# Performance work log

Measured on AMD Instinct MI355X. Metric: run time of the kernel, lower is better.

## Reference

```python
import jax, jax.numpy as jnp
import numpy as np

B, NSV, NTRK, K, H = 512, 128, 512, 8, 16


def setup_inputs() -> dict:
    key = jax.random.key(0)
    ks = jax.random.split(key, 12)
    p = lambda k, shp: (jax.random.normal(k, shp, dtype=jnp.float32) * 0.1)
    return {
        "x_sv": jax.random.normal(ks[0], (B * NSV, 2), dtype=jnp.float32),
        "x_trk": jax.random.normal(ks[1], (B * NTRK, 8), dtype=jnp.float32),
        "batch_sv": jnp.repeat(jnp.arange(B, dtype=jnp.int32), NSV),
        "batch_trk": jnp.repeat(jnp.arange(B, dtype=jnp.int32), NTRK),
        # sv_encode: Linear(2,16) -> ELU -> Linear(16,16)
        "W1s": p(ks[2], (2, H)), "b1s": jnp.zeros((H,), jnp.float32),
        "W2s": p(ks[3], (H, H)), "b2s": jnp.zeros((H,), jnp.float32),
        # trk_encode: Linear(8,16) -> ELU -> Linear(16,16)
        "W1t": p(ks[4], (8, H)), "b1t": jnp.zeros((H,), jnp.float32),
        "W2t": p(ks[5], (H, H)), "b2t": jnp.zeros((H,), jnp.float32),
        # edge MLP: Linear(2*16, 16)
        "We": p(ks[6], (2 * H, H)), "be": jnp.zeros((H,), jnp.float32),
        # output head: Linear(16, 1)
        "Wo": p(ks[7], (H, 1)), "bo": jnp.zeros((1,), jnp.float32),
    }


def reference(x_sv, x_trk, batch_sv, batch_trk,
              W1s, b1s, W2s, b2s, W1t, b1t, W2t, b2t, We, be, Wo, bo):
    # Node encoders
    sv = jax.nn.elu(x_sv @ W1s + b1s) @ W2s + b2s      # [Nsv, H]
    trk = jax.nn.elu(x_trk @ W1t + b1t) @ W2t + b2t    # [Ntrk, H]

    # Regular batching: reshape to per-event blocks (batch_sv/batch_trk are
    # contiguous repeats of arange(B) with NSV / NTRK nodes per event).
    svb = sv.reshape(B, NSV, H)      # [B, S, H]
    trkb = trk.reshape(B, NTRK, H)   # [B, T, H]

    # kNN in encoded space: squared L2 distance per event, k nearest SVs per track
    t_sq = jnp.sum(trkb * trkb, -1)[:, :, None]          # [B, T, 1]
    s_sq = jnp.sum(svb * svb, -1)[:, None, :]            # [B, 1, S]
    dots = jnp.einsum("bth,bsh->bts", trkb, svb)         # [B, T, S]
    d2 = t_sq + s_sq - 2.0 * dots                        # [B, T, S]
    _, idx = jax.lax.top_k(-d2, K)                       # [B, T, K] indices into S

    # Gather neighbor SV features: [B, T, K, H]
    nbr = jax.vmap(lambda s, i: s[i])(svb, idx)

    # EdgeConv message: nn(cat[x_i, x_j - x_i]), x_i = track (target), x_j = SV
    ti = trkb[:, :, None, :]                                    # [B, T, 1, H]
    msg_in = jnp.concatenate(
        [jnp.broadcast_to(ti, nbr.shape), nbr - ti], axis=-1)   # [B, T, K, 2H]
    msg = msg_in @ We + be                                      # [B, T, K, H]
    feats = jnp.max(msg, axis=2).reshape(B * NTRK, H)           # max aggregation

    # Output head + per-event average pool (avg_pool_x with cluster == batch)
    out = jax.nn.sigmoid(feats @ Wo + bo)                       # [Ntrk, 1]
    sums = jax.ops.segment_sum(out, batch_trk, num_segments=B)  # [B, 1]
    cnts = jax.ops.segment_sum(jnp.ones_like(out), batch_trk, num_segments=B)
    pooled = sums / cnts                                        # [B, 1]
    batch_out = jnp.arange(B, dtype=jnp.int32)
    return pooled, batch_out
```

## Files before the change

### kernel.cpp

```cpp
#include <hip/hip_runtime.h>
#include <cmath>

#define BB   512
#define NSV  128
#define NTRK 512
#define KK   8
#define HH   16
#define TPB  1024
#define RSTR 20
#define PSTR 20
#define KSTR 17

typedef float vf2 __attribute__((ext_vector_type(2)));

__device__ __forceinline__ float elu_f(float x) {
    return x > 0.0f ? x : expm1f(x);
}
__device__ __forceinline__ unsigned umin_u(unsigned a, unsigned b) { return a < b ? a : b; }
__device__ __forceinline__ unsigned med3u(unsigned a, unsigned b, unsigned c) {
    unsigned d;
    asm("v_med3_u32 %0, %1, %2, %3" : "=v"(d) : "v"(a), "v"(b), "v"(c));
    return d;
}

__global__ __launch_bounds__(TPB, 8) void fused_all(
    const float* __restrict__ x_sv, const float* __restrict__ x_trk,
    const float* __restrict__ W1s, const float* __restrict__ b1s,
    const float* __restrict__ W2s, const float* __restrict__ b2s,
    const float* __restrict__ W1t, const float* __restrict__ b1t,
    const float* __restrict__ W2t, const float* __restrict__ b2t,
    const float* __restrict__ We,  const float* __restrict__ be,
    const float* __restrict__ Wo,  const float* __restrict__ bo,
    float* __restrict__ svw,
    const float* __restrict__ svr,
    float* __restrict__ out)
{
    __shared__ float    proj[NSV][PSTR];
    __shared__ unsigned kbuf[NTRK][KSTR];
    __shared__ float    ucS[HH + 1];
    __shared__ float    sred[TPB / 64];

    const int b   = blockIdx.x, tid = threadIdx.x;
    const int tl  = tid & 511;
    const int sh  = __builtin_amdgcn_readfirstlane(tid >> 9);

    if (tid < NSV) {
        const float* xp = x_sv + (size_t)(b * NSV + tid) * 2;
        float x0 = xp[0], x1 = xp[1];
        float hb[HH];
        #pragma unroll
        for (int h = 0; h < HH; ++h)
            hb[h] = elu_f(x0 * W1s[h] + x1 * W1s[HH + h] + b1s[h]);
        float o[HH], sq = 0.0f;
        #pragma unroll
        for (int h2 = 0; h2 < HH; ++h2) {
            float a = b2s[h2];
            #pragma unroll
            for (int h = 0; h < HH; ++h) a += hb[h] * W2s[h * HH + h2];
            o[h2] = a;
            sq += a * a;
        }
        float* dst = svw + (size_t)(b * NSV + tid) * RSTR;
        #pragma unroll
        for (int h4 = 0; h4 < 4; ++h4)
            *(float4*)&dst[h4 * 4] = make_float4(o[h4*4], o[h4*4+1], o[h4*4+2], o[h4*4+3]);
        dst[HH] = 0.5f * sq;
        #pragma unroll
        for (int h = 0; h < HH; ++h) {
            float a = 0.0f;
            #pragma unroll
            for (int j = 0; j < HH; ++j) a += o[j] * We[(HH + j) * HH + h];
            proj[tid][h] = a;
        }
    } else if (tid < NSV + HH) {
        int j = tid - NSV;
        float a = 0.0f;
        #pragma unroll
        for (int h = 0; h < HH; ++h)
            a += (We[j * HH + h] - We[(HH + j) * HH + h]) * Wo[h];
        ucS[j] = a;
    } else if (tid == NSV + HH) {
        float a = bo[0];
        #pragma unroll
        for (int h = 0; h < HH; ++h) a += be[h] * Wo[h];
        ucS[HH] = a;
    }

    float tf[HH], htsq;
    vf2 ntfp[8];
    {
        const float* xp = x_trk + (size_t)(b * NTRK + tl) * 8;
        float x[8];
        *(float4*)&x[0] = *(const float4*)&xp[0];
        *(float4*)&x[4] = *(const float4*)&xp[4];
        float hb[HH];
        #pragma unroll
        for (int h = 0; h < HH; ++h) {
            float a = b1t[h];
            #pragma unroll
            for (int i = 0; i < 8; ++i) a += x[i] * W1t[i * HH + h];
            hb[h] = elu_f(a);
        }
        float sq = 0.0f;
        #pragma unroll
        for (int h2 = 0; h2 < HH; ++h2) {
            float a = b2t[h2];
            #pragma unroll
            for (int h = 0; h < HH; ++h) a += hb[h] * W2t[h * HH + h2];
            tf[h2] = a;
            sq += a * a;
        }
        htsq = 0.5f * sq;
        #pragma unroll
        for (int j = 0; j < 8; ++j) {
            vf2 t; t.x = -tf[2 * j]; t.y = -tf[2 * j + 1];
            ntfp[j] = t;
        }
    }

    unsigned k[KK];
    #pragma unroll
    for (int q = 0; q < KK; ++q) k[q] = 0xFFFFFFFFu;

    __syncthreads();

    const int sbase = sh * 64;
    const float* rp = svr + (size_t)(b * NSV + sbase) * RSTR;

    vf2 pa[8], pb[8]; float ha, hbv;

    #define LOADROW(buf, hv, idx)                                      \
        do {                                                           \
            const float* _r = rp + (size_t)(idx) * RSTR;               \
            _Pragma("unroll")                                          \
            for (int _j = 0; _j < 8; ++_j)                             \
                buf[_j] = *(const vf2*)(_r + 2 * _j);                  \
            hv = _r[HH];                                               \
        } while (0)

    #define BODY(buf, hv, idx)                                         \
        do {                                                           \
            vf2 a0 = ntfp[0] * buf[0];                                 \
            vf2 a1 = ntfp[1] * buf[1];                                 \
            vf2 a2 = ntfp[2] * buf[2];                                 \
            vf2 a3 = ntfp[3] * buf[3];                                 \
            a0 = __builtin_elementwise_fma(ntfp[4], buf[4], a0);       \
            a1 = __builtin_elementwise_fma(ntfp[5], buf[5], a1);       \
            a2 = __builtin_elementwise_fma(ntfp[6], buf[6], a2);       \
            a3 = __builtin_elementwise_fma(ntfp[7], buf[7], a3);       \
            a0 = a0 + a1; a2 = a2 + a3; a0 = a0 + a2;                  \
            float e = fmaxf((htsq + hv) + (a0.x + a0.y), 0.0f);        \
            unsigned v = (__float_as_uint(e) & 0xFFFFFF80u)            \
                         | (unsigned)(sbase + (idx));                  \
            unsigned nk0 = umin_u(v, k[0]);                            \
            unsigned nk1 = med3u(v, k[0], k[1]);                       \
            unsigned nk2 = med3u(v, k[1], k[2]);                       \
            unsigned nk3 = med3u(v, k[2], k[3]);                       \
            unsigned nk4 = med3u(v, k[3], k[4]);                       \
            unsigned nk5 = med3u(v, k[4], k[5]);                       \
            unsigned nk6 = med3u(v, k[5], k[6]);                       \
            unsigned nk7 = med3u(v, k[6], k[7]);                       \
            k[0] = nk0; k[1] = nk1; k[2] = nk2; k[3] = nk3;            \
            k[4] = nk4; k[5] = nk5; k[6] = nk6; k[7] = nk7;            \
        } while (0)

    LOADROW(pa, ha, 0);
    LOADROW(pb, hbv, 1);
    for (int s = 0; s < 64 - 2; s += 2) {
        BODY(pa, ha, s);
        LOADROW(pa, ha, s + 2);
        BODY(pb, hbv, s + 1);
        LOADROW(pb, hbv, s + 3);
    }
    BODY(pa, ha, 62);
    BODY(pb, hbv, 63);

    #undef LOADROW
    #undef BODY

    #pragma unroll
    for (int q = 0; q < KK; ++q) kbuf[tl][sh * 8 + q] = k[q];
    __syncthreads();

    unsigned m[KK];
    {
        const unsigned* pk = &kbuf[tl][(sh ^ 1) * 8];
        #pragma unroll
        for (int i = 0; i < KK; ++i) m[i] = umin_u(k[i], pk[7 - i]);
    }

    float local;
    {
        float acc = ucS[HH];
        #pragma unroll
        for (int j = 0; j < HH; ++j) acc = fmaf(tf[j], ucS[j], acc);

        float mx[HH];
        #pragma unroll
        for (int h = 0; h < HH; ++h) mx[h] = -INFINITY;
        #pragma unroll
        for (int q = 0; q < KK; ++q) {
            const float* pr = &proj[m[q] & 127u][0];
            #pragma unroll
            for (int h4 = 0; h4 < 4; ++h4) {
                float4 p = *(const float4*)&pr[h4 * 4];
                mx[h4 * 4 + 0] = fmaxf(mx[h4 * 4 + 0], p.x);
                mx[h4 * 4 + 1] = fmaxf(mx[h4 * 4 + 1], p.y);
                mx[h4 * 4 + 2] = fmaxf(mx[h4 * 4 + 2], p.z);
                mx[h4 * 4 + 3] = fmaxf(mx[h4 * 4 + 3], p.w);
            }
        }
        #pragma unroll
        for (int h = 0; h < HH; ++h) acc = fmaf(mx[h], Wo[h], acc);
        local = 1.0f / (1.0f + expf(-acc));
    }

    #pragma unroll
    for (int off = 32; off > 0; off >>= 1)
        local += __shfl_down(local, off, 64);
    if ((tid & 63) == 0) sred[tid >> 6] = local;
    __syncthreads();
    if (tid == 0) {
        float tot = 0.0f;
        #pragma unroll
        for (int w = 0; w < TPB / 64; ++w) tot += sred[w];
        out[b]      = tot * (1.0f / (2 * NTRK));
        out[BB + b] = (float)b;
    }
}

extern "C" void kernel_launch(void* const* d_in, const int* in_sizes, int n_in,
                              void* d_out, int out_size, void* d_ws, size_t ws_size,
                              hipStream_t stream) {
    const float* x_sv  = (const float*)d_in[0];
    const float* x_trk = (const float*)d_in[1];
    const float* W1s = (const float*)d_in[4];
    const float* b1s = (const float*)d_in[5];
    const float* W2s = (const float*)d_in[6];
    const float* b2s = (const float*)d_in[7];
    const float* W1t = (const float*)d_in[8];
    const float* b1t = (const float*)d_in[9];
    const float* W2t = (const float*)d_in[10];
    const float* b2t = (const float*)d_in[11];
    const float* We  = (const float*)d_in[12];
    const float* be  = (const float*)d_in[13];
    const float* Wo  = (const float*)d_in[14];
    const float* bo  = (const float*)d_in[15];
    float* out = (float*)d_out;

    float* rows = (float*)d_ws;

    fused_all<<<BB, TPB, 0, stream>>>(x_sv, x_trk,
                                      W1s, b1s, W2s, b2s,
                                      W1t, b1t, W2t, b2t,
                                      We, be, Wo, bo,
                                      rows, rows, out);
}
```

Measured before the change: 131.1 us.

## Split each event across two blocks with four SV segments and merge networks

```diff
diff --git a/kernel.cpp b/kernel.cpp
--- a/kernel.cpp
+++ b/kernel.cpp
@@ -7,9 +7,12 @@
 #define KK   8
 #define HH   16
 #define TPB  1024
+#define TRB  256
+#define SEGN 32
 #define RSTR 20
 #define PSTR 20
-#define KSTR 17
+#define TSTR 18
+#define KBS  25
 
 typedef float vf2 __attribute__((ext_vector_type(2)));
 
@@ -17,10 +20,26 @@
     return x > 0.0f ? x : expm1f(x);
 }
 __device__ __forceinline__ unsigned umin_u(unsigned a, unsigned b) { return a < b ? a : b; }
+__device__ __forceinline__ unsigned umax_u(unsigned a, unsigned b) { return a > b ? a : b; }
 __device__ __forceinline__ unsigned med3u(unsigned a, unsigned b, unsigned c) {
     unsigned d;
     asm("v_med3_u32 %0, %1, %2, %3" : "=v"(d) : "v"(a), "v"(b), "v"(c));
     return d;
+}
+__device__ __forceinline__ void ceu(unsigned& a, unsigned& b) {
+    unsigned lo = umin_u(a, b), hi = umax_u(a, b);
+    a = lo; b = hi;
+}
+__device__ __forceinline__ void merge8(unsigned* a, const unsigned* b) {
+    unsigned s[8];
+    #pragma unroll
+    for (int i = 0; i < 8; ++i) s[i] = umin_u(a[i], b[7 - i]);
+    #pragma unroll
+    for (int i = 0; i < 4; ++i) ceu(s[i], s[i + 4]);
+    ceu(s[0], s[2]); ceu(s[1], s[3]); ceu(s[4], s[6]); ceu(s[5], s[7]);
+    ceu(s[0], s[1]); ceu(s[2], s[3]); ceu(s[4], s[5]); ceu(s[6], s[7]);
+    #pragma unroll
+    for (int i = 0; i < 8; ++i) a[i] = s[i];
 }
 
 __global__ __launch_bounds__(TPB, 8) void fused_all(
@@ -33,16 +52,20 @@
     const float* __restrict__ Wo,  const float* __restrict__ bo,
     float* __restrict__ svw,
     const float* __restrict__ svr,
+    float* __restrict__ pool_g, unsigned* __restrict__ cnt_g,
     float* __restrict__ out)
 {
     __shared__ float    proj[NSV][PSTR];
-    __shared__ unsigned kbuf[NTRK][KSTR];
+    __shared__ float    tfS[TRB][TSTR];
+    __shared__ unsigned kbufS[TRB][KBS];
     __shared__ float    ucS[HH + 1];
-    __shared__ float    sred[TPB / 64];
-
-    const int b   = blockIdx.x, tid = threadIdx.x;
-    const int tl  = tid & 511;
-    const int sh  = __builtin_amdgcn_readfirstlane(tid >> 9);
+    __shared__ float    sred[4];
+
+    const int blk = blockIdx.x;
+    const int b   = blk >> 1, half = blk & 1;
+    const int tid = threadIdx.x;
+    const int tl  = tid & (TRB - 1);
+    const int seg = __builtin_amdgcn_readfirstlane(tid >> 8);
 
     if (tid < NSV) {
         const float* xp = x_sv + (size_t)(b * NSV + tid) * 2;
@@ -84,12 +107,9 @@
         #pragma unroll
         for (int h = 0; h < HH; ++h) a += be[h] * Wo[h];
         ucS[HH] = a;
-    }
-
-    float tf[HH], htsq;
-    vf2 ntfp[8];
-    {
-        const float* xp = x_trk + (size_t)(b * NTRK + tl) * 8;
+    } else if (tid >= TRB && tid < 2 * TRB) {
+        const int t = tid - TRB;
+        const float* xp = x_trk + (size_t)(b * NTRK + half * TRB + t) * 8;
         float x[8];
         *(float4*)&x[0] = *(const float4*)&xp[0];
         *(float4*)&x[4] = *(const float4*)&xp[4];
@@ -107,24 +127,28 @@
             float a = b2t[h2];
             #pragma unroll
             for (int h = 0; h < HH; ++h) a += hb[h] * W2t[h * HH + h2];
-            tf[h2] = a;
+            tfS[t][h2] = a;
             sq += a * a;
         }
-        htsq = 0.5f * sq;
-        #pragma unroll
-        for (int j = 0; j < 8; ++j) {
-            vf2 t; t.x = -tf[2 * j]; t.y = -tf[2 * j + 1];
-            ntfp[j] = t;
-        }
-    }
+        tfS[t][HH] = 0.5f * sq;
+    }
+
+    __syncthreads();
+
+    vf2 ntfp[8];
+    float htsq;
+    #pragma unroll
+    for (int j = 0; j < 8; ++j) {
+        vf2 t = *(const vf2*)&tfS[tl][2 * j];
+        ntfp[j] = -t;
+    }
+    htsq = tfS[tl][HH];
 
     unsigned k[KK];
     #pragma unroll
     for (int q = 0; q < KK; ++q) k[q] = 0xFFFFFFFFu;
 
-    __syncthreads();
-
-    const int sbase = sh * 64;
+    const int sbase = seg * SEGN;
     const float* rp = svr + (size_t)(b * NSV + sbase) * RSTR;
 
     vf2 pa[8], pb[8]; float ha, hbv;
@@ -166,35 +190,45 @@
 
     LOADROW(pa, ha, 0);
     LOADROW(pb, hbv, 1);
-    for (int s = 0; s < 64 - 2; s += 2) {
+    for (int s = 0; s < SEGN - 2; s += 2) {
         BODY(pa, ha, s);
         LOADROW(pa, ha, s + 2);
         BODY(pb, hbv, s + 1);
         LOADROW(pb, hbv, s + 3);
     }
-    BODY(pa, ha, 62);
-    BODY(pb, hbv, 63);
+    BODY(pa, ha, SEGN - 2);
+    BODY(pb, hbv, SEGN - 1);
 
     #undef LOADROW
     #undef BODY
 
-    #pragma unroll
-    for (int q = 0; q < KK; ++q) kbuf[tl][sh * 8 + q] = k[q];
+    if (seg > 0) {
+        #pragma unroll
+        for (int q = 0; q < KK; ++q) kbufS[tl][(seg - 1) * KK + q] = k[q];
+    }
     __syncthreads();
 
-    unsigned m[KK];
-    {
-        const unsigned* pk = &kbuf[tl][(sh ^ 1) * 8];
-        #pragma unroll
-        for (int i = 0; i < KK; ++i) m[i] = umin_u(k[i], pk[7 - i]);
-    }
-
-    float local;
-    {
+    float local = 0.0f;
+    if (tid < TRB) {
+        unsigned lb[KK], lc[KK], ld[KK];
+        #pragma unroll
+        for (int q = 0; q < KK; ++q) {
+            lb[q] = kbufS[tl][q];
+            lc[q] = kbufS[tl][KK + q];
+            ld[q] = kbufS[tl][2 * KK + q];
+        }
+        merge8(k, lb);
+        merge8(lc, ld);
+        unsigned m[KK];
+        #pragma unroll
+        for (int i = 0; i < KK; ++i) m[i] = umin_u(k[i], lc[7 - i]);
+
         float acc = ucS[HH];
         #pragma unroll
-        for (int j = 0; j < HH; ++j) acc = fmaf(tf[j], ucS[j], acc);
-
+        for (int j = 0; j < 8; ++j) {
+            acc = fmaf(-ntfp[j].x, ucS[2 * j],     acc);
+            acc = fmaf(-ntfp[j].y, ucS[2 * j + 1], acc);
+        }
         float mx[HH];
         #pragma unroll
         for (int h = 0; h < HH; ++h) mx[h] = -INFINITY;
@@ -213,19 +247,24 @@
         #pragma unroll
         for (int h = 0; h < HH; ++h) acc = fmaf(mx[h], Wo[h], acc);
         local = 1.0f / (1.0f + expf(-acc));
-    }
-
-    #pragma unroll
-    for (int off = 32; off > 0; off >>= 1)
-        local += __shfl_down(local, off, 64);
-    if ((tid & 63) == 0) sred[tid >> 6] = local;
+
+        #pragma unroll
+        for (int off = 32; off > 0; off >>= 1)
+            local += __shfl_down(local, off, 64);
+        if ((tid & 63) == 0) sred[tid >> 6] = local;
+    }
     __syncthreads();
+
     if (tid == 0) {
-        float tot = 0.0f;
-        #pragma unroll
-        for (int w = 0; w < TPB / 64; ++w) tot += sred[w];
-        out[b]      = tot * (1.0f / (2 * NTRK));
-        out[BB + b] = (float)b;
+        float part = sred[0] + sred[1] + sred[2] + sred[3];
+        atomicAdd(&pool_g[b], part);
+        __threadfence();
+        unsigned old = atomicAdd(&cnt_g[b], 1u);
+        if (old == 1u) {
+            float tot = atomicAdd(&pool_g[b], 0.0f);
+            out[b]      = tot * (1.0f / NTRK);
+            out[BB + b] = (float)b;
+        }
     }
 }
 
@@ -248,11 +287,15 @@
     const float* bo  = (const float*)d_in[15];
     float* out = (float*)d_out;
 
-    float* rows = (float*)d_ws;
-
-    fused_all<<<BB, TPB, 0, stream>>>(x_sv, x_trk,
-                                      W1s, b1s, W2s, b2s,
-                                      W1t, b1t, W2t, b2t,
-                                      We, be, Wo, bo,
-                                      rows, rows, out);
-}
+    float*    rows   = (float*)d_ws;
+    float*    pool_g = rows + (size_t)BB * NSV * RSTR;
+    unsigned* cnt_g  = (unsigned*)(pool_g + BB);
+
+    hipMemsetAsync(pool_g, 0, BB * (sizeof(float) + sizeof(unsigned)), stream);
+
+    fused_all<<<BB * 2, TPB, 0, stream>>>(x_sv, x_trk,
+                                          W1s, b1s, W2s, b2s,
+                                          W1t, b1t, W2t, b2t,
+                                          We, be, Wo, bo,
+                                          rows, rows, pool_g, cnt_g, out);
+}
```

Measured after the change: 156.9 us. 19.7% more time.

## Encode each track once via shared memory and halve the final merge and head work

Applied to the files above, without the earlier changes.

```diff
diff --git a/kernel.cpp b/kernel.cpp
--- a/kernel.cpp
+++ b/kernel.cpp
@@ -9,7 +9,7 @@
 #define TPB  1024
 #define RSTR 20
 #define PSTR 20
-#define KSTR 17
+#define TSTR 18
 
 typedef float vf2 __attribute__((ext_vector_type(2)));
 
@@ -36,60 +36,17 @@
     float* __restrict__ out)
 {
     __shared__ float    proj[NSV][PSTR];
-    __shared__ unsigned kbuf[NTRK][KSTR];
+    __shared__ float    tfS[NTRK][TSTR];
+    __shared__ unsigned kbuf[NTRK][KK];
     __shared__ float    ucS[HH + 1];
     __shared__ float    sred[TPB / 64];
 
     const int b   = blockIdx.x, tid = threadIdx.x;
-    const int tl  = tid & 511;
+    const int tl  = tid & (NTRK - 1);
     const int sh  = __builtin_amdgcn_readfirstlane(tid >> 9);
 
-    if (tid < NSV) {
-        const float* xp = x_sv + (size_t)(b * NSV + tid) * 2;
-        float x0 = xp[0], x1 = xp[1];
-        float hb[HH];
-        #pragma unroll
-        for (int h = 0; h < HH; ++h)
-            hb[h] = elu_f(x0 * W1s[h] + x1 * W1s[HH + h] + b1s[h]);
-        float o[HH], sq = 0.0f;
-        #pragma unroll
-        for (int h2 = 0; h2 < HH; ++h2) {
-            float a = b2s[h2];
-            #pragma unroll
-            for (int h = 0; h < HH; ++h) a += hb[h] * W2s[h * HH + h2];
-            o[h2] = a;
-            sq += a * a;
-        }
-        float* dst = svw + (size_t)(b * NSV + tid) * RSTR;
-        #pragma unroll
-        for (int h4 = 0; h4 < 4; ++h4)
-            *(float4*)&dst[h4 * 4] = make_float4(o[h4*4], o[h4*4+1], o[h4*4+2], o[h4*4+3]);
-        dst[HH] = 0.5f * sq;
-        #pragma unroll
-        for (int h = 0; h < HH; ++h) {
-            float a = 0.0f;
-            #pragma unroll
-            for (int j = 0; j < HH; ++j) a += o[j] * We[(HH + j) * HH + h];
-            proj[tid][h] = a;
-        }
-    } else if (tid < NSV + HH) {
-        int j = tid - NSV;
-        float a = 0.0f;
-        #pragma unroll
-        for (int h = 0; h < HH; ++h)
-            a += (We[j * HH + h] - We[(HH + j) * HH + h]) * Wo[h];
-        ucS[j] = a;
-    } else if (tid == NSV + HH) {
-        float a = bo[0];
-        #pragma unroll
-        for (int h = 0; h < HH; ++h) a += be[h] * Wo[h];
-        ucS[HH] = a;
-    }
-
-    float tf[HH], htsq;
-    vf2 ntfp[8];
-    {
-        const float* xp = x_trk + (size_t)(b * NTRK + tl) * 8;
+    if (tid < NTRK) {
+        const float* xp = x_trk + (size_t)(b * NTRK + tid) * 8;
         float x[8];
         *(float4*)&x[0] = *(const float4*)&xp[0];
         *(float4*)&x[4] = *(const float4*)&xp[4];
@@ -107,27 +64,72 @@
             float a = b2t[h2];
             #pragma unroll
             for (int h = 0; h < HH; ++h) a += hb[h] * W2t[h * HH + h2];
-            tf[h2] = a;
+            tfS[tid][h2] = a;
             sq += a * a;
         }
-        htsq = 0.5f * sq;
-        #pragma unroll
-        for (int j = 0; j < 8; ++j) {
-            vf2 t; t.x = -tf[2 * j]; t.y = -tf[2 * j + 1];
-            ntfp[j] = t;
-        }
-    }
+        tfS[tid][HH] = 0.5f * sq;
+    } else if (tid < NTRK + NSV) {
+        const int s = tid - NTRK;
+        const float* xp = x_sv + (size_t)(b * NSV + s) * 2;
+        float x0 = xp[0], x1 = xp[1];
+        float hb[HH];
+        #pragma unroll
+        for (int h = 0; h < HH; ++h)
+            hb[h] = elu_f(x0 * W1s[h] + x1 * W1s[HH + h] + b1s[h]);
+        float o[HH], sq = 0.0f;
+        #pragma unroll
+        for (int h2 = 0; h2 < HH; ++h2) {
+            float a = b2s[h2];
+            #pragma unroll
+            for (int h = 0; h < HH; ++h) a += hb[h] * W2s[h * HH + h2];
+            o[h2] = a;
+            sq += a * a;
+        }
+        float* dst = svw + (size_t)(b * NSV + s) * RSTR;
+        #pragma unroll
+        for (int h4 = 0; h4 < 4; ++h4)
+            *(float4*)&dst[h4 * 4] = make_float4(o[h4*4], o[h4*4+1], o[h4*4+2], o[h4*4+3]);
+        dst[HH] = 0.5f * sq;
+        #pragma unroll
+        for (int h = 0; h < HH; ++h) {
+            float a = 0.0f;
+            #pragma unroll
+            for (int j = 0; j < HH; ++j) a += o[j] * We[(HH + j) * HH + h];
+            proj[s][h] = a;
+        }
+    } else if (tid < NTRK + NSV + HH) {
+        int j = tid - NTRK - NSV;
+        float a = 0.0f;
+        #pragma unroll
+        for (int h = 0; h < HH; ++h)
+            a += (We[j * HH + h] - We[(HH + j) * HH + h]) * Wo[h];
+        ucS[j] = a;
+    } else if (tid == NTRK + NSV + HH) {
+        float a = bo[0];
+        #pragma unroll
+        for (int h = 0; h < HH; ++h) a += be[h] * Wo[h];
+        ucS[HH] = a;
+    }
+
+    __syncthreads();
+
+    vf2 ntfp[8];
+    float htsq;
+    #pragma unroll
+    for (int j = 0; j < 8; ++j) {
+        vf2 t = *(const vf2*)&tfS[tl][2 * j];
+        ntfp[j] = -t;
+    }
+    htsq = tfS[tl][HH];
 
     unsigned k[KK];
     #pragma unroll
     for (int q = 0; q < KK; ++q) k[q] = 0xFFFFFFFFu;
 
-    __syncthreads();
-
     const int sbase = sh * 64;
     const float* rp = svr + (size_t)(b * NSV + sbase) * RSTR;
 
-    vf2 pa[8], pb[8]; float ha, hbv;
+    vf2 p0[8], p1[8], p2[8]; float h0, h1, h2;
 
     #define LOADROW(buf, hv, idx)                                      \
         do {                                                           \
@@ -164,37 +166,40 @@
             k[4] = nk4; k[5] = nk5; k[6] = nk6; k[7] = nk7;            \
         } while (0)
 
-    LOADROW(pa, ha, 0);
-    LOADROW(pb, hbv, 1);
-    for (int s = 0; s < 64 - 2; s += 2) {
-        BODY(pa, ha, s);
-        LOADROW(pa, ha, s + 2);
-        BODY(pb, hbv, s + 1);
-        LOADROW(pb, hbv, s + 3);
-    }
-    BODY(pa, ha, 62);
-    BODY(pb, hbv, 63);
+    LOADROW(p0, h0, 0);
+    LOADROW(p1, h1, 1);
+    LOADROW(p2, h2, 2);
+    for (int s = 0; s < 60; s += 3) {
+        BODY(p0, h0, s);     LOADROW(p0, h0, s + 3);
+        BODY(p1, h1, s + 1); LOADROW(p1, h1, s + 4);
+        BODY(p2, h2, s + 2); LOADROW(p2, h2, s + 5);
+    }
+    BODY(p0, h0, 60); LOADROW(p0, h0, 63);
+    BODY(p1, h1, 61);
+    BODY(p2, h2, 62);
+    BODY(p0, h0, 63);
 
     #undef LOADROW
     #undef BODY
 
-    #pragma unroll
-    for (int q = 0; q < KK; ++q) kbuf[tl][sh * 8 + q] = k[q];
+    if (sh == 1) {
+        #pragma unroll
+        for (int q = 0; q < KK; ++q) kbuf[tl][q] = k[q];
+    }
     __syncthreads();
 
-    unsigned m[KK];
-    {
-        const unsigned* pk = &kbuf[tl][(sh ^ 1) * 8];
-        #pragma unroll
-        for (int i = 0; i < KK; ++i) m[i] = umin_u(k[i], pk[7 - i]);
-    }
-
-    float local;
-    {
+    float local = 0.0f;
+    if (sh == 0) {
+        unsigned m[KK];
+        #pragma unroll
+        for (int i = 0; i < KK; ++i) m[i] = umin_u(k[i], kbuf[tl][7 - i]);
+
         float acc = ucS[HH];
         #pragma unroll
-        for (int j = 0; j < HH; ++j) acc = fmaf(tf[j], ucS[j], acc);
-
+        for (int j = 0; j < 8; ++j) {
+            acc = fmaf(-ntfp[j].x, ucS[2 * j],     acc);
+            acc = fmaf(-ntfp[j].y, ucS[2 * j + 1], acc);
+        }
         float mx[HH];
         #pragma unroll
         for (int h = 0; h < HH; ++h) mx[h] = -INFINITY;
@@ -224,7 +229,7 @@
         float tot = 0.0f;
         #pragma unroll
         for (int w = 0; w < TPB / 64; ++w) tot += sred[w];
-        out[b]      = tot * (1.0f / (2 * NTRK));
+        out[b]      = tot * (1.0f / NTRK);
         out[BB + b] = (float)b;
     }
 }
```

After: 123.7 us, median of 2. -5.6%, faster.
